# Kernel optimization log

Measured on AMD Instinct MI355X. Metric: run time of the kernel, lower is better.

The kernel has to match this reference:

```python
import jax, jax.numpy as jnp
import numpy as np

B, T_DEC, T_ENC = 64, 128, 256
D_X, N_HIDDEN, N_FEED = 1024, 1024, 1024


def _glorot(key, shape):
    fan_in = shape[0]
    return jax.random.normal(key, shape, dtype=jnp.float32) / np.sqrt(fan_in)


def setup_inputs() -> dict:
    key = jax.random.key(0)
    ks = jax.random.split(key, 10)
    H = N_HIDDEN
    return {
        "x": jax.random.normal(ks[0], (B, T_DEC, D_X), dtype=jnp.float32),
        "o_enc": jax.random.normal(ks[1], (B, T_ENC, H), dtype=jnp.float32),
        "h_enc": jax.random.normal(ks[2], (B, H), dtype=jnp.float32),
        # input-feeding FFN: Dense(n_feed, tanh), input dim = n_hidden
        "Wfeed": _glorot(ks[3], (H, N_FEED)),
        "bfeed": jnp.zeros((N_FEED,), dtype=jnp.float32),
        # GRU (keras v2, reset_after=True): kernel [n_feed+d_x, 3H], recurrent [H, 3H]
        "Wx": _glorot(ks[4], (N_FEED + D_X, 3 * H)),
        "Wh": _glorot(ks[5], (H, 3 * H)),
        "bxi": jnp.zeros((3 * H,), dtype=jnp.float32),  # input bias
        "bhr": jnp.zeros((3 * H,), dtype=jnp.float32),  # recurrent bias (reset_after)
        # attention FFN: Dense(n_hidden, tanh), input dim = 2H (concat[value, h_dec])
        "Watt": _glorot(ks[6], (2 * H, H)),
        "batt": jnp.zeros((H,), dtype=jnp.float32),
    }


def reference(x, o_enc, h_enc, Wfeed, bfeed, Wx, Wh, bxi, bhr, Watt, batt):
    # x: [B, T_dec, d_x], o_enc: [B, T_enc, H], h_enc: [B, H]
    def step(carry, x_t):
        h, i_feed = carry  # h: [B,H] GRU state, i_feed: [B,H] previous attention output
        # input feeding FFN + concat with current token
        i_cat = jnp.concatenate([jnp.tanh(i_feed @ Wfeed + bfeed), x_t], axis=-1)
        # GRU cell (keras reset_after=True semantics)
        gx = i_cat @ Wx + bxi  # [B, 3H]
        gh = h @ Wh + bhr      # [B, 3H]
        xz, xr, xh = jnp.split(gx, 3, axis=-1)
        hz, hr, hh = jnp.split(gh, 3, axis=-1)
        z = jax.nn.sigmoid(xz + hz)
        r = jax.nn.sigmoid(xr + hr)
        hcand = jnp.tanh(xh + r * hh)
        h_new = z * h + (1.0 - z) * hcand  # [B, H]
        # Luong dot attention over encoder outputs
        scores = jnp.einsum('bh,bth->bt', h_new, o_enc)       # [B, T_enc]
        attn = jax.nn.softmax(scores, axis=-1)
        value = jnp.einsum('bt,bth->bh', attn, o_enc)         # [B, H]
        h_att = jnp.tanh(jnp.concatenate([value, h_new], axis=-1) @ Watt + batt)
        return (h_new, h_att), h_att

    i_feed0 = jnp.zeros_like(h_enc)
    x_t_major = jnp.swapaxes(x, 0, 1)  # [T_dec, B, d_x]
    _, outs = jax.lax.scan(step, (h_enc, i_feed0), x_t_major)
    return jnp.swapaxes(outs, 0, 1)  # [B, T_dec, H]
```

## Files before the change

### kernel.cpp

```cpp
#include <hip/hip_runtime.h>
#include <hip/hip_bf16.h>


#define NWG 256
#define NTHR 512
constexpr int BB = 64, TD = 128, TE = 256, HH = 1024, H3 = 3072;

typedef __attribute__((ext_vector_type(8))) __bf16 bf16x8;
typedef __attribute__((ext_vector_type(4))) float f32x4;
using bf = __hip_bfloat16;

__device__ __forceinline__ f32x4 mfma16(bf16x8 a, bf16x8 b, f32x4 c) {
  return __builtin_amdgcn_mfma_f32_16x16x32_bf16(a, b, c, 0, 0, 0);
}

struct Args {
  const float *x, *o_enc, *bfeed, *bxi, *bhr, *batt;
  const bf *Wf0, *Wf1, *Wf2, *Wh0, *Wh1, *Wh2;
  const bf *WxF0, *WxF1, *WxF2, *WxX0, *WxX1, *WxX2, *Wa0, *Wa1, *Wa2;
  float *h_f32;
  float *gxp;
  float *gh, *scores;
  bf *hs0, *hs1, *hs2, *ff0, *ff1, *ff2, *ifd0, *ifd1, *ifd2;
  bf *xt0, *xt1, *xt2, *vl0, *vl1, *vl2;
  unsigned *cnt, *cnt2, *go, *afl;
  float *out;
};

__device__ __forceinline__ void gbar(unsigned ep, const Args& a, int wg) {
  __syncthreads();
  if (threadIdx.x == 0) {
    __threadfence();
    unsigned* sub = a.cnt + (wg & 15) * 32;
    unsigned o = __hip_atomic_fetch_add(sub, 1u, __ATOMIC_ACQ_REL, __HIP_MEMORY_SCOPE_AGENT);
    if (o == 15) {
      __hip_atomic_store(sub, 0u, __ATOMIC_RELAXED, __HIP_MEMORY_SCOPE_AGENT);
      unsigned o2 = __hip_atomic_fetch_add(a.cnt2, 1u, __ATOMIC_ACQ_REL, __HIP_MEMORY_SCOPE_AGENT);
      if (o2 == 15) {
        __hip_atomic_store(a.cnt2, 0u, __ATOMIC_RELAXED, __HIP_MEMORY_SCOPE_AGENT);
        __hip_atomic_store(a.go, ep, __ATOMIC_RELEASE, __HIP_MEMORY_SCOPE_AGENT);
      }
    }
    while (__hip_atomic_load(a.go, __ATOMIC_RELAXED, __HIP_MEMORY_SCOPE_AGENT) < ep)
      __builtin_amdgcn_s_sleep(2);
    __threadfence();
  }
  __syncthreads();
}

__device__ __forceinline__ void split3_write(bf* p0, bf* p1, bf* p2, size_t i, float v) {
  bf b0 = __float2bfloat16(v);
  float r1 = v - __bfloat162float(b0);
  bf b1 = __float2bfloat16(r1);
  float r2 = r1 - __bfloat162float(b1);
  p0[i] = b0; p1[i] = b1; p2[i] = __float2bfloat16(r2);
}

template <int K>
__device__ __forceinline__ f32x4 gemm6(const bf* A0, const bf* A1, const bf* A2,
                                       const bf* B0, const bf* B1, const bf* B2) {
  f32x4 c0 = {0.f, 0.f, 0.f, 0.f}, c1 = c0, c2 = c0, c3 = c0;
#pragma unroll 4
  for (int k = 0; k < K; k += 32) {
    bf16x8 a0 = *(const bf16x8*)(A0 + k);
    bf16x8 a1 = *(const bf16x8*)(A1 + k);
    bf16x8 a2 = *(const bf16x8*)(A2 + k);
    bf16x8 b0 = *(const bf16x8*)(B0 + k);
    bf16x8 b1 = *(const bf16x8*)(B1 + k);
    bf16x8 b2 = *(const bf16x8*)(B2 + k);
    c0 = mfma16(a0, b0, c0);
    c1 = mfma16(a0, b1, c1);
    c2 = mfma16(a1, b0, c2);
    c3 = mfma16(a1, b1, c3);
    c0 = mfma16(a0, b2, c0);
    c1 = mfma16(a2, b0, c1);
  }
  f32x4 s;
#pragma unroll
  for (int i = 0; i < 4; ++i) s[i] = (c0[i] + c1[i]) + (c2[i] + c3[i]);
  return s;
}

__global__ __launch_bounds__(NTHR, 2) void decoder_main(Args a) {
  const int wg = blockIdx.x;
  const int tid = threadIdx.x;
  const int lane = tid & 63;
  const int wv = tid >> 6;
  const int lrow = lane & 15;
  const int lkg = lane >> 4;

  __shared__ float s_acc[2][4][16][16];
  __shared__ float s_h[HH];
  __shared__ float s_sm[TE];
  __shared__ float s_red[8];
  __shared__ float s_val[2][256];

  unsigned ep = 0;

  for (int t = 0; t < TD; ++t) {
    {
      const bool isf = (wg < 64);
      const int j0 = (isf ? wg : wg - 64) * 16;
      const bf* A0 = isf ? a.ifd0 : a.hs0;
      const bf* A1 = isf ? a.ifd1 : a.hs1;
      const bf* A2 = isf ? a.ifd2 : a.hs2;
      const bf* B0 = isf ? a.Wf0 : a.Wh0;
      const bf* B1 = isf ? a.Wf1 : a.Wh1;
      const bf* B2 = isf ? a.Wf2 : a.Wh2;
      const int mt = wv & 3, kh = wv >> 2;
      const size_t aoff = (size_t)(mt * 16 + lrow) * HH + kh * 512 + lkg * 8;
      const size_t boff = (size_t)(j0 + lrow) * HH + kh * 512 + lkg * 8;
      f32x4 acc = gemm6<512>(A0 + aoff, A1 + aoff, A2 + aoff, B0 + boff, B1 + boff, B2 + boff);
#pragma unroll
      for (int r = 0; r < 4; ++r) s_acc[kh][mt][lkg * 4 + r][lrow] = acc[r];
      __syncthreads();
#pragma unroll
      for (int e = tid; e < 1024; e += NTHR) {
        const int row = e >> 4, c = e & 15;
        const int emt = row >> 4, err2 = row & 15;
        float v = s_acc[0][emt][err2][c] + s_acc[1][emt][err2][c];
        const int col = j0 + c;
        if (isf) {
          float f = tanhf(v + a.bfeed[col]);
          split3_write(a.ff0, a.ff1, a.ff2, (size_t)row * HH + col, f);
        } else {
          a.gh[(size_t)row * H3 + col] = v + a.bhr[col];
        }
      }
    }
    gbar(++ep, a, wg);

    if (wv < 6) {
      const int unit = wg * 6 + wv;
      const int kh2 = unit & 1;
      const int jt = (unit >> 1) & 63;
      const int gm = unit >> 7;
      const int g = gm >> 2, mt = gm & 3;
      const bf* A0 = kh2 ? a.xt0 : a.ff0;
      const bf* A1 = kh2 ? a.xt1 : a.ff1;
      const bf* A2 = kh2 ? a.xt2 : a.ff2;
      const bf* B0 = kh2 ? a.WxX0 : a.WxF0;
      const bf* B1 = kh2 ? a.WxX1 : a.WxF1;
      const bf* B2 = kh2 ? a.WxX2 : a.WxF2;
      const size_t aoff = (size_t)(mt * 16 + lrow) * HH + lkg * 8;
      const size_t boff = (size_t)(g * HH + jt * 16 + lrow) * HH + lkg * 8;
      f32x4 acc = gemm6<1024>(A0 + aoff, A1 + aoff, A2 + aoff, B0 + boff, B1 + boff, B2 + boff);
      const int gcol = g * 1024 + jt * 16 + lrow;
#pragma unroll
      for (int r = 0; r < 4; ++r)
        a.gxp[(size_t)(kh2 * 64 + mt * 16 + lkg * 4 + r) * H3 + gcol] = acc[r];
    }
    gbar(++ep, a, wg);

    {
      const int b = wg >> 2, q = wg & 3;
      const float* hold = a.h_f32 + (size_t)(t & 1) * (BB * HH);
      float* hnew = a.h_f32 + (size_t)((t + 1) & 1) * (BB * HH);
      const float* ghb = a.gh + (size_t)b * H3;
#pragma unroll
      for (int ii = 0; ii < 2; ++ii) {
        const int col = ii * NTHR + tid;
        const float* g0 = a.gxp + (size_t)b * H3;
        const float* g1 = a.gxp + (size_t)(64 + b) * H3;
        float gz = a.bxi[col] + g0[col] + g1[col];
        float gr = a.bxi[HH + col] + g0[HH + col] + g1[HH + col];
        float gc = a.bxi[2 * HH + col] + g0[2 * HH + col] + g1[2 * HH + col];
        float z = 1.f / (1.f + expf(-(gz + ghb[col])));
        float rr = 1.f / (1.f + expf(-(gr + ghb[HH + col])));
        float hc = tanhf(gc + rr * ghb[2 * HH + col]);
        float hn = z * hold[(size_t)b * HH + col] + (1.f - z) * hc;
        s_h[col] = hn;
        if (q == 0) {
          hnew[(size_t)b * HH + col] = hn;
          split3_write(a.hs0, a.hs1, a.hs2, (size_t)b * HH + col, hn);
        }
      }
      __syncthreads();
      {
        f32x4 sh0 = *(const f32x4*)(s_h + 0 + lane * 4);
        f32x4 sh1 = *(const f32x4*)(s_h + 256 + lane * 4);
        f32x4 sh2 = *(const f32x4*)(s_h + 512 + lane * 4);
        f32x4 sh3 = *(const f32x4*)(s_h + 768 + lane * 4);
        const float* obase = a.o_enc + ((size_t)b * TE + q * 64 + wv * 8) * HH + lane * 4;
#pragma unroll 2
        for (int i = 0; i < 8; ++i) {
          const float* orow = obase + (size_t)i * HH;
          f32x4 o0 = *(const f32x4*)(orow);
          f32x4 o1 = *(const f32x4*)(orow + 256);
          f32x4 o2 = *(const f32x4*)(orow + 512);
          f32x4 o3 = *(const f32x4*)(orow + 768);
          float s = o0[0] * sh0[0] + o0[1] * sh0[1] + o0[2] * sh0[2] + o0[3] * sh0[3]
                  + o1[0] * sh1[0] + o1[1] * sh1[1] + o1[2] * sh1[2] + o1[3] * sh1[3]
                  + o2[0] * sh2[0] + o2[1] * sh2[1] + o2[2] * sh2[2] + o2[3] * sh2[3]
                  + o3[0] * sh3[0] + o3[1] * sh3[1] + o3[2] * sh3[2] + o3[3] * sh3[3];
          for (int off = 32; off; off >>= 1) s += __shfl_xor(s, off);
          if (lane == 0) a.scores[(size_t)b * TE + q * 64 + wv * 8 + i] = s;
        }
      }
      __syncthreads();
      if (tid == 0) {
        __threadfence();
        __hip_atomic_store(&a.afl[b * 4 + q], (unsigned)(t + 1),
                           __ATOMIC_RELEASE, __HIP_MEMORY_SCOPE_AGENT);
        for (int p = 1; p < 4; ++p) {
          unsigned idx = b * 4 + ((q + p) & 3);
          while (__hip_atomic_load(&a.afl[idx], __ATOMIC_RELAXED, __HIP_MEMORY_SCOPE_AGENT)
                 < (unsigned)(t + 1))
            __builtin_amdgcn_s_sleep(1);
        }
        __threadfence();
      }
      __syncthreads();
      float sc = 0.f, p = 0.f;
      if (tid < 256) {
        sc = a.scores[(size_t)b * TE + tid];
        float v = sc;
        for (int off = 32; off; off >>= 1) v = fmaxf(v, __shfl_xor(v, off));
        if (lane == 0) s_red[wv] = v;
      }
      __syncthreads();
      {
        float mx = fmaxf(fmaxf(s_red[0], s_red[1]), fmaxf(s_red[2], s_red[3]));
        if (tid < 256) {
          p = expf(sc - mx);
          float sum = p;
          for (int off = 32; off; off >>= 1) sum += __shfl_xor(sum, off);
          if (lane == 0) s_red[4 + wv] = sum;
        }
      }
      __syncthreads();
      if (tid < 256) {
        float tot = s_red[4] + s_red[5] + s_red[6] + s_red[7];
        s_sm[tid] = p / tot;
      }
      __syncthreads();
      {
        const int c = tid & 255, th = tid >> 8;
        const int j = q * 256 + c;
        const float* ob = a.o_enc + (size_t)b * TE * HH + j;
        float accv = 0.f;
        for (int tt2 = th * 128; tt2 < th * 128 + 128; ++tt2) {
          float w2 = s_sm[tt2];
          if (w2 > 1e-8f) accv += w2 * ob[(size_t)tt2 * HH];
        }
        s_val[th][c] = accv;
      }
      __syncthreads();
      if (tid < 256)
        split3_write(a.vl0, a.vl1, a.vl2, (size_t)b * HH + q * 256 + tid,
                     s_val[0][tid] + s_val[1][tid]);
    }
    gbar(++ep, a, wg);

    {
      const int kq8 = wv;
      const int cu = wg & 63;
      const int mt = wg >> 6;
      const bool isv = (kq8 < 4);
      const int koff = (kq8 & 3) * 256;
      const bf* A0 = isv ? a.vl0 : a.hs0;
      const bf* A1 = isv ? a.vl1 : a.hs1;
      const bf* A2 = isv ? a.vl2 : a.hs2;
      const size_t aoff = (size_t)(mt * 16 + lrow) * HH + koff + lkg * 8;
      const size_t boff = (size_t)(cu * 16 + lrow) * 2048 + kq8 * 256 + lkg * 8;
      f32x4 acc = gemm6<256>(A0 + aoff, A1 + aoff, A2 + aoff,
                             a.Wa0 + boff, a.Wa1 + boff, a.Wa2 + boff);
#pragma unroll
      for (int r = 0; r < 4; ++r)
        a.gxp[(size_t)(kq8 * 64 + mt * 16 + lkg * 4 + r) * 1024 + cu * 16 + lrow] = acc[r];
    }
    gbar(++ep, a, wg);

    {
      const int id = wg * NTHR + tid;
      if (id < 65536) {
        const int row = id >> 10, col = id & 1023;
        float s = a.batt[col];
#pragma unroll
        for (int kq = 0; kq < 8; ++kq) s += a.gxp[(size_t)(kq * 64 + row) * 1024 + col];
        float hv = tanhf(s);
        a.out[((size_t)row * TD + t) * HH + col] = hv;
        split3_write(a.ifd0, a.ifd1, a.ifd2, (size_t)row * HH + col, hv);
      } else if (t + 1 < TD) {
        const int id2 = id - 65536;
        const int row = id2 >> 10, col = id2 & 1023;
        split3_write(a.xt0, a.xt1, a.xt2, (size_t)id2,
                     a.x[((size_t)row * TD + (t + 1)) * HH + col]);
      }
    }
    gbar(++ep, a, wg);
  }
}

__global__ void k_tr3(const float* src, bf* d0, bf* d1, bf* d2, int R, int C) {
  __shared__ float tile[32][33];
  int c0 = blockIdx.x * 32, r0 = blockIdx.y * 32;
  int tx = threadIdx.x & 31, ty = threadIdx.x >> 5;
  for (int i = ty; i < 32; i += 8)
    tile[i][tx] = src[(size_t)(r0 + i) * C + c0 + tx];
  __syncthreads();
  for (int i = ty; i < 32; i += 8) {
    float v = tile[tx][i];
    size_t o = (size_t)(c0 + i) * R + r0 + tx;
    bf b0 = __float2bfloat16(v);
    float r1 = v - __bfloat162float(b0);
    bf b1 = __float2bfloat16(r1);
    d0[o] = b0; d1[o] = b1; d2[o] = __float2bfloat16(r1 - __bfloat162float(b1));
  }
}

__global__ void k_init(const float* h_enc, float* h_f32, bf* h0, bf* h1, bf* h2,
                       bf* i0, bf* i1, bf* i2, const float* x, bf* x0, bf* x1, bf* x2) {
  int i = blockIdx.x * blockDim.x + threadIdx.x;
  float v = h_enc[i];
  h_f32[i] = v;
  split3_write(h0, h1, h2, i, v);
  bf z = __float2bfloat16(0.f);
  i0[i] = z; i1[i] = z; i2[i] = z;
  int row = i >> 10, col = i & 1023;
  split3_write(x0, x1, x2, i, x[((size_t)row * TD + 0) * HH + col]);
}

extern "C" void kernel_launch(void* const* d_in, const int* in_sizes, int n_in,
                              void* d_out, int out_size, void* d_ws, size_t ws_size,
                              hipStream_t stream) {
  const float* x     = (const float*)d_in[0];
  const float* o_enc = (const float*)d_in[1];
  const float* h_enc = (const float*)d_in[2];
  const float* Wfeed = (const float*)d_in[3];
  const float* bfeed = (const float*)d_in[4];
  const float* Wx    = (const float*)d_in[5];
  const float* Wh    = (const float*)d_in[6];
  const float* bxi   = (const float*)d_in[7];
  const float* bhr   = (const float*)d_in[8];
  const float* Watt  = (const float*)d_in[9];
  const float* batt  = (const float*)d_in[10];

  char* w = (char*)d_ws;
  auto alloc = [&](size_t b) { char* p = w; w += (b + 255) & ~255ULL; return p; };

  const size_t M1 = (size_t)1024 * 1024 * 2;
  bf* Wf[3];  for (auto& p : Wf)  p = (bf*)alloc(M1);
  bf* Wh_[3]; for (auto& p : Wh_) p = (bf*)alloc(3 * M1);
  bf* WxF[3]; for (auto& p : WxF) p = (bf*)alloc(3 * M1);
  bf* WxX[3]; for (auto& p : WxX) p = (bf*)alloc(3 * M1);
  bf* Wa[3];  for (auto& p : Wa)  p = (bf*)alloc(2 * M1);
  float* h_f32  = (float*)alloc((size_t)2 * BB * HH * 4);
  float* gxp    = (float*)alloc((size_t)8 * BB * H3 * 4);
  float* gh     = (float*)alloc((size_t)BB * H3 * 4);
  float* scores = (float*)alloc((size_t)BB * TE * 4);
  const size_t AB = (size_t)BB * HH * 2;
  bf *hs[3], *ff[3], *ifd[3], *xt[3], *vl[3];
  for (auto& p : hs)  p = (bf*)alloc(AB);
  for (auto& p : ff)  p = (bf*)alloc(AB);
  for (auto& p : ifd) p = (bf*)alloc(AB);
  for (auto& p : xt)  p = (bf*)alloc(AB);
  for (auto& p : vl)  p = (bf*)alloc(AB);
  unsigned* flags = (unsigned*)alloc(8192);

  hipMemsetAsync(flags, 0, 8192, stream);
  k_tr3<<<dim3(32, 32), 256, 0, stream>>>(Wfeed, Wf[0], Wf[1], Wf[2], 1024, 1024);
  k_tr3<<<dim3(96, 32), 256, 0, stream>>>(Wx, WxF[0], WxF[1], WxF[2], 1024, 3072);
  k_tr3<<<dim3(96, 32), 256, 0, stream>>>(Wx + (size_t)1024 * 3072, WxX[0], WxX[1], WxX[2], 1024, 3072);
  k_tr3<<<dim3(96, 32), 256, 0, stream>>>(Wh, Wh_[0], Wh_[1], Wh_[2], 1024, 3072);
  k_tr3<<<dim3(32, 64), 256, 0, stream>>>(Watt, Wa[0], Wa[1], Wa[2], 2048, 1024);
  k_init<<<BB * HH / 256, 256, 0, stream>>>(h_enc, h_f32, hs[0], hs[1], hs[2],
                                            ifd[0], ifd[1], ifd[2], x, xt[0], xt[1], xt[2]);

  Args a;
  a.x = x; a.o_enc = o_enc; a.bfeed = bfeed; a.bxi = bxi; a.bhr = bhr; a.batt = batt;
  a.Wf0 = Wf[0]; a.Wf1 = Wf[1]; a.Wf2 = Wf[2];
  a.Wh0 = Wh_[0]; a.Wh1 = Wh_[1]; a.Wh2 = Wh_[2];
  a.WxF0 = WxF[0]; a.WxF1 = WxF[1]; a.WxF2 = WxF[2];
  a.WxX0 = WxX[0]; a.WxX1 = WxX[1]; a.WxX2 = WxX[2];
  a.Wa0 = Wa[0]; a.Wa1 = Wa[1]; a.Wa2 = Wa[2];
  a.h_f32 = h_f32; a.gxp = gxp; a.gh = gh; a.scores = scores;
  a.hs0 = hs[0]; a.hs1 = hs[1]; a.hs2 = hs[2];
  a.ff0 = ff[0]; a.ff1 = ff[1]; a.ff2 = ff[2];
  a.ifd0 = ifd[0]; a.ifd1 = ifd[1]; a.ifd2 = ifd[2];
  a.xt0 = xt[0]; a.xt1 = xt[1]; a.xt2 = xt[2];
  a.vl0 = vl[0]; a.vl1 = vl[1]; a.vl2 = vl[2];
  a.cnt = flags; a.cnt2 = flags + 512; a.go = flags + 544; a.afl = flags + 576;
  a.out = (float*)d_out;

  decoder_main<<<NWG, NTHR, 0, stream>>>(a);
}
```

Measured before the change: 24.12 ms.

## Double workgroup threads, deepen split-K across GEMM phases, prefetch encoder rows

Raises the persistent kernel from 512 to 1024 threads per workgroup. Each GEMM phase gets finer split-K: feed and recurrent GEMMs go 2-way to 4-way, the GRU input GEMM goes 2-way to 4-way, and the attention GEMM goes 8-way to 16-way, with the reductions widened to match. Idle waves in the GRU input phase now touch this workgroup's o_enc slice, which looks meant to warm cache before the attention score phase. The batch-to-workgroup mapping changes to wg&63 so the prefetching workgroup matches the consumer. This adds more partial-sum traffic and higher register pressure from the 1024-thread launch bound.

New measurement: 34.88 ms. +44.6%, slower.

```diff
diff --git a/kernel.cpp b/kernel.cpp
--- a/kernel.cpp
+++ b/kernel.cpp
@@ -3,7 +3,7 @@
 
 
 #define NWG 256
-#define NTHR 512
+#define NTHR 1024
 constexpr int BB = 64, TD = 128, TE = 256, HH = 1024, H3 = 3072;
 
 typedef __attribute__((ext_vector_type(8))) __bf16 bf16x8;
@@ -81,7 +81,7 @@
   return s;
 }
 
-__global__ __launch_bounds__(NTHR, 2) void decoder_main(Args a) {
+__global__ __launch_bounds__(NTHR, 4) void decoder_main(Args a) {
   const int wg = blockIdx.x;
   const int tid = threadIdx.x;
   const int lane = tid & 63;
@@ -89,7 +89,7 @@
   const int lrow = lane & 15;
   const int lkg = lane >> 4;
 
-  __shared__ float s_acc[2][4][16][16];
+  __shared__ float s_acc[4][4][16][16];
   __shared__ float s_h[HH];
   __shared__ float s_sm[TE];
   __shared__ float s_red[8];
@@ -107,18 +107,18 @@
       const bf* B0 = isf ? a.Wf0 : a.Wh0;
       const bf* B1 = isf ? a.Wf1 : a.Wh1;
       const bf* B2 = isf ? a.Wf2 : a.Wh2;
-      const int mt = wv & 3, kh = wv >> 2;
-      const size_t aoff = (size_t)(mt * 16 + lrow) * HH + kh * 512 + lkg * 8;
-      const size_t boff = (size_t)(j0 + lrow) * HH + kh * 512 + lkg * 8;
-      f32x4 acc = gemm6<512>(A0 + aoff, A1 + aoff, A2 + aoff, B0 + boff, B1 + boff, B2 + boff);
+      const int mt = wv >> 2, kq = wv & 3;
+      const size_t aoff = (size_t)(mt * 16 + lrow) * HH + kq * 256 + lkg * 8;
+      const size_t boff = (size_t)(j0 + lrow) * HH + kq * 256 + lkg * 8;
+      f32x4 acc = gemm6<256>(A0 + aoff, A1 + aoff, A2 + aoff, B0 + boff, B1 + boff, B2 + boff);
 #pragma unroll
-      for (int r = 0; r < 4; ++r) s_acc[kh][mt][lkg * 4 + r][lrow] = acc[r];
-      __syncthreads();
-#pragma unroll
-      for (int e = tid; e < 1024; e += NTHR) {
-        const int row = e >> 4, c = e & 15;
-        const int emt = row >> 4, err2 = row & 15;
-        float v = s_acc[0][emt][err2][c] + s_acc[1][emt][err2][c];
+      for (int r = 0; r < 4; ++r) s_acc[kq][mt][lkg * 4 + r][lrow] = acc[r];
+      __syncthreads();
+      {
+        const int row = tid >> 4, c = tid & 15;
+        const int emt = row >> 4, r2 = row & 15;
+        float v = (s_acc[0][emt][r2][c] + s_acc[1][emt][r2][c]) +
+                  (s_acc[2][emt][r2][c] + s_acc[3][emt][r2][c]);
         const int col = j0 + c;
         if (isf) {
           float f = tanhf(v + a.bfeed[col]);
@@ -130,11 +130,12 @@
     }
     gbar(++ep, a, wg);
 
-    if (wv < 6) {
-      const int unit = wg * 6 + wv;
-      const int kh2 = unit & 1;
-      const int jt = (unit >> 1) & 63;
-      const int gm = unit >> 7;
+    if (wv < 12) {
+      const int unit = wg * 12 + wv;
+      const int kq2 = unit & 1;
+      const int kh2 = (unit >> 1) & 1;
+      const int jt = (unit >> 2) & 63;
+      const int gm = unit >> 8;
       const int g = gm >> 2, mt = gm & 3;
       const bf* A0 = kh2 ? a.xt0 : a.ff0;
       const bf* A1 = kh2 ? a.xt1 : a.ff1;
@@ -142,29 +143,47 @@
       const bf* B0 = kh2 ? a.WxX0 : a.WxF0;
       const bf* B1 = kh2 ? a.WxX1 : a.WxF1;
       const bf* B2 = kh2 ? a.WxX2 : a.WxF2;
-      const size_t aoff = (size_t)(mt * 16 + lrow) * HH + lkg * 8;
-      const size_t boff = (size_t)(g * HH + jt * 16 + lrow) * HH + lkg * 8;
-      f32x4 acc = gemm6<1024>(A0 + aoff, A1 + aoff, A2 + aoff, B0 + boff, B1 + boff, B2 + boff);
+      const size_t aoff = (size_t)(mt * 16 + lrow) * HH + kq2 * 512 + lkg * 8;
+      const size_t boff = (size_t)(g * HH + jt * 16 + lrow) * HH + kq2 * 512 + lkg * 8;
+      f32x4 acc = gemm6<512>(A0 + aoff, A1 + aoff, A2 + aoff, B0 + boff, B1 + boff, B2 + boff);
+      const int p = kh2 * 2 + kq2;
       const int gcol = g * 1024 + jt * 16 + lrow;
 #pragma unroll
       for (int r = 0; r < 4; ++r)
-        a.gxp[(size_t)(kh2 * 64 + mt * 16 + lkg * 4 + r) * H3 + gcol] = acc[r];
+        a.gxp[(size_t)(p * 64 + mt * 16 + lkg * 4 + r) * H3 + gcol] = acc[r];
+    } else {
+      const int b3 = wg & 63, q3 = wg >> 6;
+      const int pw = wv - 12;
+      const float* pbase = a.o_enc + ((size_t)b3 * TE + q3 * 64 + pw * 16) * HH + lane * 4;
+      float pf = 0.f;
+      for (int rr = 0; rr < 16; ++rr) {
+        const float* prow = pbase + (size_t)rr * HH;
+        f32x4 v0 = *(const f32x4*)(prow);
+        f32x4 v1 = *(const f32x4*)(prow + 256);
+        f32x4 v2 = *(const f32x4*)(prow + 512);
+        f32x4 v3 = *(const f32x4*)(prow + 768);
+        pf += v0[0] + v1[0] + v2[0] + v3[0];
+      }
+      asm volatile("" :: "v"(pf));
     }
     gbar(++ep, a, wg);
 
     {
-      const int b = wg >> 2, q = wg & 3;
+      const int b = wg & 63, q = wg >> 6;
       const float* hold = a.h_f32 + (size_t)(t & 1) * (BB * HH);
       float* hnew = a.h_f32 + (size_t)((t + 1) & 1) * (BB * HH);
       const float* ghb = a.gh + (size_t)b * H3;
-#pragma unroll
-      for (int ii = 0; ii < 2; ++ii) {
-        const int col = ii * NTHR + tid;
-        const float* g0 = a.gxp + (size_t)b * H3;
-        const float* g1 = a.gxp + (size_t)(64 + b) * H3;
-        float gz = a.bxi[col] + g0[col] + g1[col];
-        float gr = a.bxi[HH + col] + g0[HH + col] + g1[HH + col];
-        float gc = a.bxi[2 * HH + col] + g0[2 * HH + col] + g1[2 * HH + col];
+      {
+        const int col = tid;
+        const float* g0 = a.gxp + (size_t)(0 * 64 + b) * H3;
+        const float* g1 = a.gxp + (size_t)(1 * 64 + b) * H3;
+        const float* g2 = a.gxp + (size_t)(2 * 64 + b) * H3;
+        const float* g3 = a.gxp + (size_t)(3 * 64 + b) * H3;
+        float gz = a.bxi[col] + ((g0[col] + g1[col]) + (g2[col] + g3[col]));
+        float gr = a.bxi[HH + col] +
+                   ((g0[HH + col] + g1[HH + col]) + (g2[HH + col] + g3[HH + col]));
+        float gc = a.bxi[2 * HH + col] + ((g0[2 * HH + col] + g1[2 * HH + col]) +
+                                          (g2[2 * HH + col] + g3[2 * HH + col]));
         float z = 1.f / (1.f + expf(-(gz + ghb[col])));
         float rr = 1.f / (1.f + expf(-(gr + ghb[HH + col])));
         float hc = tanhf(gc + rr * ghb[2 * HH + col]);
@@ -181,9 +200,9 @@
         f32x4 sh1 = *(const f32x4*)(s_h + 256 + lane * 4);
         f32x4 sh2 = *(const f32x4*)(s_h + 512 + lane * 4);
         f32x4 sh3 = *(const f32x4*)(s_h + 768 + lane * 4);
-        const float* obase = a.o_enc + ((size_t)b * TE + q * 64 + wv * 8) * HH + lane * 4;
+        const float* obase = a.o_enc + ((size_t)b * TE + q * 64 + wv * 4) * HH + lane * 4;
 #pragma unroll 2
-        for (int i = 0; i < 8; ++i) {
+        for (int i = 0; i < 4; ++i) {
           const float* orow = obase + (size_t)i * HH;
           f32x4 o0 = *(const f32x4*)(orow);
           f32x4 o1 = *(const f32x4*)(orow + 256);
@@ -194,7 +213,7 @@
                   + o2[0] * sh2[0] + o2[1] * sh2[1] + o2[2] * sh2[2] + o2[3] * sh2[3]
                   + o3[0] * sh3[0] + o3[1] * sh3[1] + o3[2] * sh3[2] + o3[3] * sh3[3];
           for (int off = 32; off; off >>= 1) s += __shfl_xor(s, off);
-          if (lane == 0) a.scores[(size_t)b * TE + q * 64 + wv * 8 + i] = s;
+          if (lane == 0) a.scores[(size_t)b * TE + q * 64 + wv * 4 + i] = s;
         }
       }
       __syncthreads();
@@ -234,7 +253,7 @@
         s_sm[tid] = p / tot;
       }
       __syncthreads();
-      {
+      if (tid < 512) {
         const int c = tid & 255, th = tid >> 8;
         const int j = q * 256 + c;
         const float* ob = a.o_enc + (size_t)b * TE * HH + j;
@@ -253,21 +272,21 @@
     gbar(++ep, a, wg);
 
     {
-      const int kq8 = wv;
       const int cu = wg & 63;
       const int mt = wg >> 6;
-      const bool isv = (kq8 < 4);
-      const int koff = (kq8 & 3) * 256;
+      const int kq16 = wv;
+      const bool isv = (kq16 < 8);
+      const int koff = (kq16 & 7) * 128;
       const bf* A0 = isv ? a.vl0 : a.hs0;
       const bf* A1 = isv ? a.vl1 : a.hs1;
       const bf* A2 = isv ? a.vl2 : a.hs2;
       const size_t aoff = (size_t)(mt * 16 + lrow) * HH + koff + lkg * 8;
-      const size_t boff = (size_t)(cu * 16 + lrow) * 2048 + kq8 * 256 + lkg * 8;
-      f32x4 acc = gemm6<256>(A0 + aoff, A1 + aoff, A2 + aoff,
+      const size_t boff = (size_t)(cu * 16 + lrow) * 2048 + kq16 * 128 + lkg * 8;
+      f32x4 acc = gemm6<128>(A0 + aoff, A1 + aoff, A2 + aoff,
                              a.Wa0 + boff, a.Wa1 + boff, a.Wa2 + boff);
 #pragma unroll
       for (int r = 0; r < 4; ++r)
-        a.gxp[(size_t)(kq8 * 64 + mt * 16 + lkg * 4 + r) * 1024 + cu * 16 + lrow] = acc[r];
+        a.gxp[(size_t)(kq16 * 64 + mt * 16 + lkg * 4 + r) * 1024 + cu * 16 + lrow] = acc[r];
     }
     gbar(++ep, a, wg);
 
@@ -277,11 +296,11 @@
         const int row = id >> 10, col = id & 1023;
         float s = a.batt[col];
 #pragma unroll
-        for (int kq = 0; kq < 8; ++kq) s += a.gxp[(size_t)(kq * 64 + row) * 1024 + col];
+        for (int kq = 0; kq < 16; ++kq) s += a.gxp[(size_t)(kq * 64 + row) * 1024 + col];
         float hv = tanhf(s);
         a.out[((size_t)row * TD + t) * HH + col] = hv;
         split3_write(a.ifd0, a.ifd1, a.ifd2, (size_t)row * HH + col, hv);
-      } else if (t + 1 < TD) {
+      } else if (id < 131072 && t + 1 < TD) {
         const int id2 = id - 65536;
         const int row = id2 >> 10, col = id2 & 1023;
         split3_write(a.xt0, a.xt1, a.xt2, (size_t)id2,
@@ -346,7 +365,7 @@
   bf* WxX[3]; for (auto& p : WxX) p = (bf*)alloc(3 * M1);
   bf* Wa[3];  for (auto& p : Wa)  p = (bf*)alloc(2 * M1);
   float* h_f32  = (float*)alloc((size_t)2 * BB * HH * 4);
-  float* gxp    = (float*)alloc((size_t)8 * BB * H3 * 4);
+  float* gxp    = (float*)alloc((size_t)16 * BB * 1024 * 4);
   float* gh     = (float*)alloc((size_t)BB * H3 * 4);
   float* scores = (float*)alloc((size_t)BB * TE * 4);
   const size_t AB = (size_t)BB * HH * 2;
```

## Stage GEMM operands and encoder rows through LDS with async global-to-LDS loads

Applied to the files above, without the earlier changes.

Replaces the direct register loads in the split-bf16 MFMA GEMMs with a double-buffered global_load_lds pipeline per wave, using explicit vmcnt/lgkmcnt waits. The attention score pass now streams encoder rows into a 96KB LDS arena the same way. The score pass also remaps batch/quarter assignment across workgroups and shrinks the unused part of a scratch buffer. The aim is to overlap memory latency with MFMA work in this latency-bound persistent kernel. The cost is extra LDS traffic, more block-wide barriers inside the score loop, and lower possible occupancy from the large LDS footprint.

Result: slower. 33.80 ms (+40.1%).

```diff
diff --git a/kernel.cpp b/kernel.cpp
--- a/kernel.cpp
+++ b/kernel.cpp
@@ -12,6 +12,28 @@
 
 __device__ __forceinline__ f32x4 mfma16(bf16x8 a, bf16x8 b, f32x4 c) {
   return __builtin_amdgcn_mfma_f32_16x16x32_bf16(a, b, c, 0, 0, 0);
+}
+
+__device__ __forceinline__ void dma16(const void* g, void* l) {
+  __builtin_amdgcn_global_load_lds(
+      (const __attribute__((address_space(1))) void*)g,
+      (__attribute__((address_space(3))) void*)l, 16, 0, 0);
+}
+__device__ __forceinline__ void wait_vm6() {
+  asm volatile("s_waitcnt vmcnt(6)" ::: "memory");
+  __builtin_amdgcn_sched_barrier(0);
+}
+__device__ __forceinline__ void wait_vm4() {
+  asm volatile("s_waitcnt vmcnt(4)" ::: "memory");
+  __builtin_amdgcn_sched_barrier(0);
+}
+__device__ __forceinline__ void wait_vm0() {
+  asm volatile("s_waitcnt vmcnt(0)" ::: "memory");
+  __builtin_amdgcn_sched_barrier(0);
+}
+__device__ __forceinline__ void wait_lgkm0() {
+  asm volatile("s_waitcnt lgkmcnt(0)" ::: "memory");
+  __builtin_amdgcn_sched_barrier(0);
 }
 
 struct Args {
@@ -56,18 +78,43 @@
   p0[i] = b0; p1[i] = b1; p2[i] = __float2bfloat16(r2);
 }
 
-template <int K>
-__device__ __forceinline__ f32x4 gemm6(const bf* A0, const bf* A1, const bf* A2,
-                                       const bf* B0, const bf* B1, const bf* B2) {
+template <int KB>
+__device__ __forceinline__ f32x4 gemm6_dma(const bf* A0, const bf* A1, const bf* A2,
+                                           const bf* B0, const bf* B1, const bf* B2,
+                                           int sA, int sB, char* scr) {
+  const int lane = threadIdx.x & 63;
+  const size_t ao = (size_t)(lane & 15) * sA + (lane >> 4) * 8;
+  const size_t bo = (size_t)(lane & 15) * sB + (lane >> 4) * 8;
+  const bf* s0 = A0 + ao;
+  const bf* s1 = A1 + ao;
+  const bf* s2 = A2 + ao;
+  const bf* s3 = B0 + bo;
+  const bf* s4 = B1 + bo;
+  const bf* s5 = B2 + bo;
+  auto issue = [&](int kb, int ring) {
+    char* d = scr + ring * 6144;
+    dma16(s0 + kb * 32, d);
+    dma16(s1 + kb * 32, d + 1024);
+    dma16(s2 + kb * 32, d + 2048);
+    dma16(s3 + kb * 32, d + 3072);
+    dma16(s4 + kb * 32, d + 4096);
+    dma16(s5 + kb * 32, d + 5120);
+  };
+  issue(0, 0);
+  issue(1, 1);
   f32x4 c0 = {0.f, 0.f, 0.f, 0.f}, c1 = c0, c2 = c0, c3 = c0;
-#pragma unroll 4
-  for (int k = 0; k < K; k += 32) {
-    bf16x8 a0 = *(const bf16x8*)(A0 + k);
-    bf16x8 a1 = *(const bf16x8*)(A1 + k);
-    bf16x8 a2 = *(const bf16x8*)(A2 + k);
-    bf16x8 b0 = *(const bf16x8*)(B0 + k);
-    bf16x8 b1 = *(const bf16x8*)(B1 + k);
-    bf16x8 b2 = *(const bf16x8*)(B2 + k);
+  const int lb = lane * 16;
+  for (int kb = 0; kb < KB; ++kb) {
+    if (kb + 1 < KB) wait_vm6(); else wait_vm0();
+    const char* d = scr + (kb & 1) * 6144;
+    bf16x8 a0 = *(const bf16x8*)(d + lb);
+    bf16x8 a1 = *(const bf16x8*)(d + 1024 + lb);
+    bf16x8 a2 = *(const bf16x8*)(d + 2048 + lb);
+    bf16x8 b0 = *(const bf16x8*)(d + 3072 + lb);
+    bf16x8 b1 = *(const bf16x8*)(d + 4096 + lb);
+    bf16x8 b2 = *(const bf16x8*)(d + 5120 + lb);
+    wait_lgkm0();
+    if (kb + 2 < KB) issue(kb + 2, kb & 1);
     c0 = mfma16(a0, b0, c0);
     c1 = mfma16(a0, b1, c1);
     c2 = mfma16(a1, b0, c2);
@@ -89,6 +136,7 @@
   const int lrow = lane & 15;
   const int lkg = lane >> 4;
 
+  __shared__ char s_arena[98304];
   __shared__ float s_acc[2][4][16][16];
   __shared__ float s_h[HH];
   __shared__ float s_sm[TE];
@@ -108,17 +156,19 @@
       const bf* B1 = isf ? a.Wf1 : a.Wh1;
       const bf* B2 = isf ? a.Wf2 : a.Wh2;
       const int mt = wv & 3, kh = wv >> 2;
-      const size_t aoff = (size_t)(mt * 16 + lrow) * HH + kh * 512 + lkg * 8;
-      const size_t boff = (size_t)(j0 + lrow) * HH + kh * 512 + lkg * 8;
-      f32x4 acc = gemm6<512>(A0 + aoff, A1 + aoff, A2 + aoff, B0 + boff, B1 + boff, B2 + boff);
+      const size_t ab = (size_t)(mt * 16) * HH + kh * 512;
+      const size_t bb = (size_t)j0 * HH + kh * 512;
+      f32x4 acc = gemm6_dma<16>(A0 + ab, A1 + ab, A2 + ab,
+                                B0 + bb, B1 + bb, B2 + bb,
+                                HH, HH, s_arena + wv * 12288);
 #pragma unroll
       for (int r = 0; r < 4; ++r) s_acc[kh][mt][lkg * 4 + r][lrow] = acc[r];
       __syncthreads();
 #pragma unroll
       for (int e = tid; e < 1024; e += NTHR) {
         const int row = e >> 4, c = e & 15;
-        const int emt = row >> 4, err2 = row & 15;
-        float v = s_acc[0][emt][err2][c] + s_acc[1][emt][err2][c];
+        const int emt = row >> 4, r2 = row & 15;
+        float v = s_acc[0][emt][r2][c] + s_acc[1][emt][r2][c];
         const int col = j0 + c;
         if (isf) {
           float f = tanhf(v + a.bfeed[col]);
@@ -142,9 +192,11 @@
       const bf* B0 = kh2 ? a.WxX0 : a.WxF0;
       const bf* B1 = kh2 ? a.WxX1 : a.WxF1;
       const bf* B2 = kh2 ? a.WxX2 : a.WxF2;
-      const size_t aoff = (size_t)(mt * 16 + lrow) * HH + lkg * 8;
-      const size_t boff = (size_t)(g * HH + jt * 16 + lrow) * HH + lkg * 8;
-      f32x4 acc = gemm6<1024>(A0 + aoff, A1 + aoff, A2 + aoff, B0 + boff, B1 + boff, B2 + boff);
+      const size_t ab = (size_t)(mt * 16) * HH;
+      const size_t bb = (size_t)(g * HH + jt * 16) * HH;
+      f32x4 acc = gemm6_dma<32>(A0 + ab, A1 + ab, A2 + ab,
+                                B0 + bb, B1 + bb, B2 + bb,
+                                HH, HH, s_arena + wv * 12288);
       const int gcol = g * 1024 + jt * 16 + lrow;
 #pragma unroll
       for (int r = 0; r < 4; ++r)
@@ -153,7 +205,7 @@
     gbar(++ep, a, wg);
 
     {
-      const int b = wg >> 2, q = wg & 3;
+      const int b = wg & 63, q = wg >> 6;
       const float* hold = a.h_f32 + (size_t)(t & 1) * (BB * HH);
       float* hnew = a.h_f32 + (size_t)((t + 1) & 1) * (BB * HH);
       const float* ghb = a.gh + (size_t)b * H3;
@@ -181,23 +233,34 @@
         f32x4 sh1 = *(const f32x4*)(s_h + 256 + lane * 4);
         f32x4 sh2 = *(const f32x4*)(s_h + 512 + lane * 4);
         f32x4 sh3 = *(const f32x4*)(s_h + 768 + lane * 4);
-        const float* obase = a.o_enc + ((size_t)b * TE + q * 64 + wv * 8) * HH + lane * 4;
-#pragma unroll 2
-        for (int i = 0; i < 8; ++i) {
-          const float* orow = obase + (size_t)i * HH;
-          f32x4 o0 = *(const f32x4*)(orow);
-          f32x4 o1 = *(const f32x4*)(orow + 256);
-          f32x4 o2 = *(const f32x4*)(orow + 512);
-          f32x4 o3 = *(const f32x4*)(orow + 768);
+        const float* obase = a.o_enc + ((size_t)b * TE + q * 64) * HH;
+        auto sc_issue = [&](int c, int ring) {
+          const char* src = (const char*)(obase + (size_t)(c * 8 + wv) * HH) + lane * 16;
+          char* d = s_arena + ring * 32768 + wv * 4096;
+          dma16(src, d);
+          dma16(src + 1024, d + 1024);
+          dma16(src + 2048, d + 2048);
+          dma16(src + 3072, d + 3072);
+        };
+        sc_issue(0, 0);
+        for (int c = 0; c < 8; ++c) {
+          if (c + 1 < 8) { sc_issue(c + 1, (c + 1) & 1); wait_vm4(); }
+          else wait_vm0();
+          __syncthreads();
+          const float* row = (const float*)(s_arena + (c & 1) * 32768 + wv * 4096);
+          f32x4 o0 = *(const f32x4*)(row + lane * 4);
+          f32x4 o1 = *(const f32x4*)(row + 256 + lane * 4);
+          f32x4 o2 = *(const f32x4*)(row + 512 + lane * 4);
+          f32x4 o3 = *(const f32x4*)(row + 768 + lane * 4);
           float s = o0[0] * sh0[0] + o0[1] * sh0[1] + o0[2] * sh0[2] + o0[3] * sh0[3]
                   + o1[0] * sh1[0] + o1[1] * sh1[1] + o1[2] * sh1[2] + o1[3] * sh1[3]
                   + o2[0] * sh2[0] + o2[1] * sh2[1] + o2[2] * sh2[2] + o2[3] * sh2[3]
                   + o3[0] * sh3[0] + o3[1] * sh3[1] + o3[2] * sh3[2] + o3[3] * sh3[3];
           for (int off = 32; off; off >>= 1) s += __shfl_xor(s, off);
-          if (lane == 0) a.scores[(size_t)b * TE + q * 64 + wv * 8 + i] = s;
-        }
-      }
-      __syncthreads();
+          if (lane == 0) a.scores[(size_t)b * TE + q * 64 + c * 8 + wv] = s;
+          __syncthreads();
+        }
+      }
       if (tid == 0) {
         __threadfence();
         __hip_atomic_store(&a.afl[b * 4 + q], (unsigned)(t + 1),
@@ -253,18 +316,19 @@
     gbar(++ep, a, wg);
 
     {
-      const int kq8 = wv;
       const int cu = wg & 63;
       const int mt = wg >> 6;
+      const int kq8 = wv;
       const bool isv = (kq8 < 4);
       const int koff = (kq8 & 3) * 256;
       const bf* A0 = isv ? a.vl0 : a.hs0;
       const bf* A1 = isv ? a.vl1 : a.hs1;
       const bf* A2 = isv ? a.vl2 : a.hs2;
-      const size_t aoff = (size_t)(mt * 16 + lrow) * HH + koff + lkg * 8;
-      const size_t boff = (size_t)(cu * 16 + lrow) * 2048 + kq8 * 256 + lkg * 8;
-      f32x4 acc = gemm6<256>(A0 + aoff, A1 + aoff, A2 + aoff,
-                             a.Wa0 + boff, a.Wa1 + boff, a.Wa2 + boff);
+      const size_t ab = (size_t)(mt * 16) * HH + koff;
+      const size_t bb = (size_t)(cu * 16) * 2048 + kq8 * 256;
+      f32x4 acc = gemm6_dma<8>(A0 + ab, A1 + ab, A2 + ab,
+                               a.Wa0 + bb, a.Wa1 + bb, a.Wa2 + bb,
+                               HH, 2048, s_arena + wv * 12288);
 #pragma unroll
       for (int r = 0; r < 4; ++r)
         a.gxp[(size_t)(kq8 * 64 + mt * 16 + lkg * 4 + r) * 1024 + cu * 16 + lrow] = acc[r];
@@ -346,7 +410,7 @@
   bf* WxX[3]; for (auto& p : WxX) p = (bf*)alloc(3 * M1);
   bf* Wa[3];  for (auto& p : Wa)  p = (bf*)alloc(2 * M1);
   float* h_f32  = (float*)alloc((size_t)2 * BB * HH * 4);
-  float* gxp    = (float*)alloc((size_t)8 * BB * H3 * 4);
+  float* gxp    = (float*)alloc((size_t)8 * BB * 1024 * 4);
   float* gh     = (float*)alloc((size_t)BB * H3 * 4);
   float* scores = (float*)alloc((size_t)BB * TE * 4);
   const size_t AB = (size_t)BB * HH * 2;
```
